# Kernel optimization log

Hardware: AMD Instinct MI355X
Metric: run time of the kernel (lower is better)

## Reference

```python
import jax, jax.numpy as jnp
import numpy as np

N, E = 50000, 800000
D, H, C, ED = 128, 8, 16, 4  # embed_dim, heads, head_dim, edge_dim


def _add_self_loops(edge_index, ea, n):
    # PyG add_self_loops with fill_value='mean': self-loop edge_attr is the
    # mean of incoming edge attributes per destination node (0 if none).
    src, dst = edge_index[0], edge_index[1]
    deg = jax.ops.segment_sum(jnp.ones((src.shape[0],), ea.dtype), dst, num_segments=n)
    loop_ea = jax.ops.segment_sum(ea, dst, num_segments=n) / jnp.maximum(deg, 1.0)[:, None]
    ar = jnp.arange(n, dtype=src.dtype)
    return (jnp.concatenate([src, ar]), jnp.concatenate([dst, ar]),
            jnp.concatenate([ea, loop_ea], axis=0))


def _gatv2(x, src, dst, ea, Wl, bl, Wr, br, We, att, bias, concat):
    n = x.shape[0]
    xl = (x @ Wl + bl).reshape(n, H, C)   # lin_l -> messages (source)
    xr = (x @ Wr + br).reshape(n, H, C)   # lin_r -> target
    e = (ea @ We).reshape(-1, H, C)       # lin_edge (no bias in PyG)
    m = jax.nn.leaky_relu(xl[src] + xr[dst] + e, negative_slope=0.2)  # [Etot,H,C]
    alpha = jnp.einsum('ehc,hc->eh', m, att)
    amax = jax.ops.segment_max(alpha, dst, num_segments=n)   # every node has a self loop
    ex = jnp.exp(alpha - amax[dst])
    den = jax.ops.segment_sum(ex, dst, num_segments=n)
    a = ex / den[dst]                                        # segment softmax over dst
    out = jax.ops.segment_sum(xl[src] * a[:, :, None], dst, num_segments=n)  # [N,H,C]
    out = out.reshape(n, H * C) if concat else out.mean(axis=1)
    return out + bias


def _ln(h, g, b):
    mu = h.mean(-1, keepdims=True)
    var = jnp.var(h, axis=-1, keepdims=True)
    return (h - mu) / jnp.sqrt(var + 1e-5) * g + b


def setup_inputs() -> dict:
    key = jax.random.key(0)
    ks = jax.random.split(key, 32)
    s = 0.05
    inp = {
        'x': jax.random.normal(ks[0], (N, D), jnp.float32),
        'edge_index': jax.random.randint(ks[1], (2, E), 0, N, jnp.int32),
        'edge_attr': jax.random.normal(ks[2], (E, ED), jnp.float32),
    }
    dims = [(D, H * C), (H * C, H * C), (H * C, C)]  # (in_dim, bias_dim per layer)
    k = 3
    for i, (din, bdim) in enumerate(dims):
        inp[f'Wl{i}'] = jax.random.normal(ks[k], (din, H * C), jnp.float32) * s; k += 1
        inp[f'bl{i}'] = jnp.zeros((H * C,), jnp.float32)
        inp[f'Wr{i}'] = jax.random.normal(ks[k], (din, H * C), jnp.float32) * s; k += 1
        inp[f'br{i}'] = jnp.zeros((H * C,), jnp.float32)
        inp[f'We{i}'] = jax.random.normal(ks[k], (ED, H * C), jnp.float32) * s; k += 1
        inp[f'att{i}'] = jax.random.normal(ks[k], (H, C), jnp.float32) * s; k += 1
        inp[f'b{i}'] = jnp.zeros((bdim,), jnp.float32)
        inp[f'g{i}'] = jnp.ones((bdim,), jnp.float32)
        inp[f'be{i}'] = jnp.zeros((bdim,), jnp.float32)
    inp['Wout'] = jax.random.normal(ks[k], (C, D), jnp.float32) * s
    inp['bout'] = jnp.zeros((D,), jnp.float32)
    return inp


def reference(x, edge_index, edge_attr,
              Wl0, bl0, Wr0, br0, We0, att0, b0, g0, be0,
              Wl1, bl1, Wr1, br1, We1, att1, b1, g1, be1,
              Wl2, bl2, Wr2, br2, We2, att2, b2, g2, be2,
              Wout, bout):
    n = x.shape[0]
    src, dst, ea = _add_self_loops(edge_index, edge_attr, n)
    layers = [
        (Wl0, bl0, Wr0, br0, We0, att0, b0, g0, be0, True),
        (Wl1, bl1, Wr1, br1, We1, att1, b1, g1, be1, True),
        (Wl2, bl2, Wr2, br2, We2, att2, b2, g2, be2, False),
    ]
    for (Wl, bl, Wr, br, We, att, bias, g, be, concat) in layers:
        h = _gatv2(x, src, dst, ea, Wl, bl, Wr, br, We, att, bias, concat)
        h = jax.nn.elu(h)
        h = _ln(h, g, be)
        if h.shape == x.shape:  # residual (layers 0,1)
            h = h + x
        x = h
    return x @ Wout + bout
```

## Files before the change

### kernel.cpp

```cpp
#include <hip/hip_runtime.h>
#include <hip/hip_bf16.h>

#define ND 128
#define NH 8
#define NC 16

typedef float v2f __attribute__((ext_vector_type(2)));
typedef short bf16x8 __attribute__((ext_vector_type(8)));
typedef float f32x4 __attribute__((ext_vector_type(4)));

static inline size_t alignup(size_t x){ return (x + 255) & ~size_t(255); }

__device__ __forceinline__ ushort f2bf(float f){
    __hip_bfloat16 h = __float2bfloat16(f);
    return *reinterpret_cast<ushort*>(&h);
}

__device__ __forceinline__ v2f unpack_bf2(uint u){
    v2f r;
    r.x = __uint_as_float(u << 16);
    r.y = __uint_as_float(u & 0xffff0000u);
    return r;
}

__device__ __forceinline__ v2f lrelu2(v2f z){
    v2f s = z * 0.2f;
    v2f r;
    r.x = fmaxf(z.x, s.x);
    r.y = fmaxf(z.y, s.y);
    return r;
}

__device__ __forceinline__ float hred8(float x){
    int y;
    y = __builtin_amdgcn_mov_dpp(__float_as_int(x), 0xB1, 0xF, 0xF, true);
    x += __int_as_float(y);
    y = __builtin_amdgcn_mov_dpp(__float_as_int(x), 0x4E, 0xF, 0xF, true);
    x += __int_as_float(y);
    y = __builtin_amdgcn_mov_dpp(__float_as_int(x), 0x141, 0xF, 0xF, true);
    x += __int_as_float(y);
    return x;
}


struct WSrc { const float* p[6]; };

#define WTHREADS (6 * 16384)

__global__ void prep_kernel(WSrc s, ushort* __restrict__ wt,
                            const int* __restrict__ dsts, int* __restrict__ deg, int E)
{
    int id = blockIdx.x * blockDim.x + threadIdx.x;
    if (id < WTHREADS) {
        int m = id >> 14;
        int r = id & 16383;
        int n = r >> 7, k = r & 127;
        wt[(size_t)m * 16384 + n * 128 + k] = f2bf(s.p[m][k * 128 + n]);
    } else {
        int e4 = (id - WTHREADS) * 4;
        if (e4 + 3 < E) {
            int4 d = *(const int4*)(dsts + e4);
            atomicAdd(&deg[d.x], 1);
            atomicAdd(&deg[d.y], 1);
            atomicAdd(&deg[d.z], 1);
            atomicAdd(&deg[d.w], 1);
        } else if (e4 < E) {
            for (int e = e4; e < E; ++e) atomicAdd(&deg[dsts[e]], 1);
        }
    }
}

__global__ __launch_bounds__(1024) void scan_kernel(const int* __restrict__ deg,
                                                    int* __restrict__ rowstart, int n)
{
    __shared__ int wsum[16];
    int tid = threadIdx.x;
    int lane = tid & 63, wid = tid >> 6;
    int carry = 0;
    for (int base = 0; base < n; base += 4096) {
        int idx = base + tid * 4;
        int4 d = make_int4(0, 0, 0, 0);
        if (idx + 3 < n) d = *(const int4*)(deg + idx);
        else {
            if (idx < n)     d.x = deg[idx];
            if (idx + 1 < n) d.y = deg[idx + 1];
            if (idx + 2 < n) d.z = deg[idx + 2];
        }
        int p0 = (d.x + 3) & ~3, p1 = (d.y + 3) & ~3;
        int p2 = (d.z + 3) & ~3, p3 = (d.w + 3) & ~3;
        int tsum = p0 + p1 + p2 + p3;
        int s = tsum;
        #pragma unroll
        for (int o = 1; o < 64; o <<= 1) {
            int t = __shfl_up(s, o);
            if (lane >= o) s += t;
        }
        if (lane == 63) wsum[wid] = s;
        __syncthreads();
        int off = carry;
        #pragma unroll
        for (int w = 0; w < 16; ++w) {
            int ws_ = wsum[w];
            if (w < wid) off += ws_;
        }
        int total = 0;
        #pragma unroll
        for (int w = 0; w < 16; ++w) total += wsum[w];
        int excl = off + (s - tsum);
        if (idx < n)     rowstart[idx]     = excl;
        if (idx + 1 < n) rowstart[idx + 1] = excl + p0;
        if (idx + 2 < n) rowstart[idx + 2] = excl + p0 + p1;
        if (idx + 3 < n) rowstart[idx + 3] = excl + p0 + p1 + p2;
        carry += total;
        __syncthreads();
    }
    if (tid == 0) rowstart[n] = carry;
}

__global__ void scatter_kernel(const int* __restrict__ srcs, const int* __restrict__ dsts,
                               const float4* __restrict__ ea4,
                               const int* __restrict__ rowstart, const int* __restrict__ deg,
                               int* __restrict__ cursor, uint4* __restrict__ recs, int E, int n)
{
    int id = blockIdx.x * blockDim.x + threadIdx.x;
    if (id < E) {
        int d = dsts[id];
        int pos = rowstart[d] + atomicAdd(&cursor[d], 1);
        float4 a = ea4[id];
        recs[pos] = make_uint4((uint)(srcs[id] << 8),
                               (uint)f2bf(a.x) | ((uint)f2bf(a.y) << 16),
                               (uint)f2bf(a.z) | ((uint)f2bf(a.w) << 16), 0u);
    } else if (id < E + n) {
        int v = id - E;
        int d = deg[v];
        int p = rowstart[v] + d;
        int pe = rowstart[v] + ((d + 3) & ~3);
        for (; p < pe; ++p) recs[p] = make_uint4(0u, 0u, 0u, 0u);
    } else if (id < E + n + 96) {
        int p = rowstart[n] + (id - E - n);
        recs[p] = make_uint4(0u, 0u, 0u, 0u);
    }
}

__global__ void easum_kernel(const int* __restrict__ rowstart, const int* __restrict__ deg,
                             const uint4* __restrict__ recs, float4* __restrict__ easum, int n)
{
    int v = blockIdx.x * blockDim.x + threadIdx.x;
    if (v >= n) return;
    int p0 = rowstart[v], d = deg[v];
    float sx = 0.f, sy = 0.f, sz = 0.f, sw = 0.f;
    for (int p = p0; p < p0 + d; ++p) {
        uint4 a = recs[p];
        sx += __uint_as_float(a.y << 16);
        sy += __uint_as_float(a.y & 0xffff0000u);
        sz += __uint_as_float(a.z << 16);
        sw += __uint_as_float(a.z & 0xffff0000u);
    }
    float inv = 1.0f / (float)(d > 0 ? d : 1);
    easum[v] = make_float4(sx * inv, sy * inv, sz * inv, sw * inv);
}


__global__ __launch_bounds__(256) void gemm_mfma(
    const float* __restrict__ X,
    const ushort* __restrict__ WTl, const float* __restrict__ bl,
    const ushort* __restrict__ WTr, const float* __restrict__ br,
    ushort* __restrict__ XLB, ushort* __restrict__ XRB, int nrows)
{
    __shared__ ushort xhi[64][136];
    __shared__ ushort xlo[64][136];
    int tid = threadIdx.x;
    int row0 = blockIdx.x * 64;

    const float4* X4 = (const float4*)X;
    #pragma unroll
    for (int i = tid; i < 64*32; i += 256) {
        int r = i >> 5, c = i & 31;
        float4 v = make_float4(0.f, 0.f, 0.f, 0.f);
        if (row0 + r < nrows) v = X4[(size_t)(row0 + r) * 32 + c];
        ushort4 h, l;
        h.x = f2bf(v.x); l.x = f2bf(v.x - __uint_as_float((uint)h.x << 16));
        h.y = f2bf(v.y); l.y = f2bf(v.y - __uint_as_float((uint)h.y << 16));
        h.z = f2bf(v.z); l.z = f2bf(v.z - __uint_as_float((uint)h.z << 16));
        h.w = f2bf(v.w); l.w = f2bf(v.w - __uint_as_float((uint)h.w << 16));
        *(ushort4*)&xhi[r][c * 4] = h;
        *(ushort4*)&xlo[r][c * 4] = l;
    }
    __syncthreads();

    int lane = tid & 63;
    int wid = tid >> 6;
    int c15 = lane & 15;
    int kblk = lane >> 4;
    int rowb = wid * 16;

    f32x4 accl[8], accr[8];
    #pragma unroll
    for (int nt = 0; nt < 8; ++nt) {
        float bvl = bl[nt * 16 + c15];
        float bvr = br[nt * 16 + c15];
        accl[nt] = (f32x4){bvl, bvl, bvl, bvl};
        accr[nt] = (f32x4){bvr, bvr, bvr, bvr};
    }

    const bf16x8* WL8 = (const bf16x8*)WTl;
    const bf16x8* WR8 = (const bf16x8*)WTr;

    #pragma unroll
    for (int kc = 0; kc < 4; ++kc) {
        int k0 = kc * 32 + kblk * 8;
        bf16x8 ahi = *(const bf16x8*)&xhi[rowb + c15][k0];
        bf16x8 alo = *(const bf16x8*)&xlo[rowb + c15][k0];
        int kidx = k0 >> 3;
        #pragma unroll
        for (int nt = 0; nt < 8; ++nt) {
            int bi = (nt * 16 + c15) * 16 + kidx;
            bf16x8 bfl = WL8[bi];
            bf16x8 bfr = WR8[bi];
            accl[nt] = __builtin_amdgcn_mfma_f32_16x16x32_bf16(ahi, bfl, accl[nt], 0, 0, 0);
            accl[nt] = __builtin_amdgcn_mfma_f32_16x16x32_bf16(alo, bfl, accl[nt], 0, 0, 0);
            accr[nt] = __builtin_amdgcn_mfma_f32_16x16x32_bf16(ahi, bfr, accr[nt], 0, 0, 0);
            accr[nt] = __builtin_amdgcn_mfma_f32_16x16x32_bf16(alo, bfr, accr[nt], 0, 0, 0);
        }
    }

    int crow = rowb + (lane >> 4) * 4;
    #pragma unroll
    for (int j = 0; j < 4; ++j) {
        int row = row0 + crow + j;
        if (row < nrows) {
            #pragma unroll
            for (int nt = 0; nt < 8; ++nt) {
                XLB[(size_t)row * 128 + nt * 16 + c15] = f2bf(accl[nt][j]);
                XRB[(size_t)row * 128 + nt * 16 + c15] = f2bf(accr[nt][j]);
            }
        }
    }
}


__device__ __forceinline__ void gat_wave(
    int dstv, int t,
    const uint* __restrict__ xl_u, const uint* __restrict__ xr_u,
    const int* __restrict__ rowstart, const int* __restrict__ deg,
    const uint4* __restrict__ recs, const float4* __restrict__ easum,
    const float* __restrict__ We, const float* __restrict__ att,
    v2f& r_out, float& l_out)
{
    v2f we0  = ((const v2f*)(We))[t];
    v2f we1  = ((const v2f*)(We + ND))[t];
    v2f we2  = ((const v2f*)(We + 2*ND))[t];
    v2f we3  = ((const v2f*)(We + 3*ND))[t];
    v2f attv = ((const v2f*)att)[t] * 1.44269504f;
    v2f xrv  = unpack_bf2(xr_u[(((uint)dstv) << 6) + t]);

    int p0 = __builtin_amdgcn_readfirstlane(rowstart[dstv]);
    int dv = __builtin_amdgcn_readfirstlane(deg[dstv]);
    int nb = (dv + 3) >> 2;

    uint xsw = xl_u[(((uint)dstv) << 6) + t];

    const uint4* rp = recs + p0;
    const char* xlc = (const char*)xl_u;
    uint t4 = (uint)t * 4u;

    v2f a = {0.f, 0.f};
    float lsum = 0.f;

    uint4 rA0 = rp[0],  rA1 = rp[1],  rA2 = rp[2],  rA3 = rp[3];
    uint4 rB0 = rp[4],  rB1 = rp[5],  rB2 = rp[6],  rB3 = rp[7];
    uint4 rC0 = rp[8],  rC1 = rp[9],  rC2 = rp[10], rC3 = rp[11];
    uint xA0 = *(const uint*)(xlc + (rA0.x + t4));
    uint xA1 = *(const uint*)(xlc + (rA1.x + t4));
    uint xA2 = *(const uint*)(xlc + (rA2.x + t4));
    uint xA3 = *(const uint*)(xlc + (rA3.x + t4));
    uint xB0 = *(const uint*)(xlc + (rB0.x + t4));
    uint xB1 = *(const uint*)(xlc + (rB1.x + t4));
    uint xB2 = *(const uint*)(xlc + (rB2.x + t4));
    uint xB3 = *(const uint*)(xlc + (rB3.x + t4));

    for (int ib = 0; ib < nb; ++ib) {
        uint xC0 = *(const uint*)(xlc + (rC0.x + t4));
        uint xC1 = *(const uint*)(xlc + (rC1.x + t4));
        uint xC2 = *(const uint*)(xlc + (rC2.x + t4));
        uint xC3 = *(const uint*)(xlc + (rC3.x + t4));
        uint4 rD0 = rp[ib*4 + 12], rD1 = rp[ib*4 + 13];
        uint4 rD2 = rp[ib*4 + 14], rD3 = rp[ib*4 + 15];

        float e0x = __uint_as_float(rA0.y << 16), e0y = __uint_as_float(rA0.y & 0xffff0000u);
        float e0z = __uint_as_float(rA0.z << 16), e0w = __uint_as_float(rA0.z & 0xffff0000u);
        float e1x = __uint_as_float(rA1.y << 16), e1y = __uint_as_float(rA1.y & 0xffff0000u);
        float e1z = __uint_as_float(rA1.z << 16), e1w = __uint_as_float(rA1.z & 0xffff0000u);
        float e2x = __uint_as_float(rA2.y << 16), e2y = __uint_as_float(rA2.y & 0xffff0000u);
        float e2z = __uint_as_float(rA2.z << 16), e2w = __uint_as_float(rA2.z & 0xffff0000u);
        float e3x = __uint_as_float(rA3.y << 16), e3y = __uint_as_float(rA3.y & 0xffff0000u);
        float e3z = __uint_as_float(rA3.z << 16), e3w = __uint_as_float(rA3.z & 0xffff0000u);

        v2f b0 = xrv + we0*e0x + we1*e0y + we2*e0z + we3*e0w;
        v2f b1 = xrv + we0*e1x + we1*e1y + we2*e1z + we3*e1w;
        v2f b2 = xrv + we0*e2x + we1*e2y + we2*e2z + we3*e2w;
        v2f b3 = xrv + we0*e3x + we1*e3y + we2*e3z + we3*e3w;

        v2f x0 = unpack_bf2(xA0);
        v2f x1 = unpack_bf2(xA1);
        v2f x2 = unpack_bf2(xA2);
        v2f x3 = unpack_bf2(xA3);

        v2f l0 = lrelu2(x0 + b0);
        v2f l1 = lrelu2(x1 + b1);
        v2f l2 = lrelu2(x2 + b2);
        v2f l3 = lrelu2(x3 + b3);

        v2f q0 = l0 * attv;
        v2f q1 = l1 * attv;
        v2f q2 = l2 * attv;
        v2f q3 = l3 * attv;
        float pt0 = q0.x + q0.y;
        float pt1 = q1.x + q1.y;
        float pt2 = q2.x + q2.y;
        float pt3 = q3.x + q3.y;

        if (ib == nb - 1) {
            int live = dv - ib*4;
            pt1 = (live > 1) ? pt1 : -1e30f;
            pt2 = (live > 2) ? pt2 : -1e30f;
            pt3 = (live > 3) ? pt3 : -1e30f;
        }

        float al0 = hred8(pt0);
        float al1 = hred8(pt1);
        float al2 = hred8(pt2);
        float al3 = hred8(pt3);

        float pe0 = exp2f(al0);
        float pe1 = exp2f(al1);
        float pe2 = exp2f(al2);
        float pe3 = exp2f(al3);
        lsum += (pe0 + pe1) + (pe2 + pe3);
        a += x0 * pe0;
        a += x1 * pe1;
        a += x2 * pe2;
        a += x3 * pe3;

        xA0 = xB0; xA1 = xB1; xA2 = xB2; xA3 = xB3;
        xB0 = xC0; xB1 = xC1; xB2 = xC2; xB3 = xC3;
        rA0 = rB0; rA1 = rB1; rA2 = rB2; rA3 = rB3;
        rB0 = rC0; rB1 = rC1; rB2 = rC2; rB3 = rC3;
        rC0 = rD0; rC1 = rD1; rC2 = rD2; rC3 = rD3;
    }

    float4 em = easum[dstv];
    v2f xs = unpack_bf2(xsw);
    v2f bs = xrv + we0*em.x + we1*em.y + we2*em.z + we3*em.w;
    v2f ls = lrelu2(xs + bs);
    v2f qs = ls * attv;
    float al = hred8(qs.x + qs.y);
    float pe = exp2f(al);
    l_out = lsum + pe;
    r_out = a + xs * pe;
}

__global__ __launch_bounds__(256) void attn_concat(
    const ushort* __restrict__ xlb, const ushort* __restrict__ xrb,
    const float* __restrict__ xin,
    const int* __restrict__ rowstart, const int* __restrict__ deg,
    const uint4* __restrict__ recs, const float4* __restrict__ easum,
    const float* __restrict__ We, const float* __restrict__ att,
    const float* __restrict__ bias, const float* __restrict__ g, const float* __restrict__ be,
    float* __restrict__ out, int n)
{
    int wid = threadIdx.x >> 6;
    int t = threadIdx.x & 63;
    int dstv = blockIdx.x * 4 + wid;
    if (dstv >= n) return;

    v2f av; float l;
    gat_wave(dstv, t, (const uint*)xlb, (const uint*)xrb, rowstart, deg, recs, easum,
             We, att, av, l);

    v2f bv = ((const v2f*)bias)[t];
    float linv = 1.0f / l;
    v2f h = av * linv + bv;
    h.x = h.x > 0.f ? h.x : (__expf(h.x) - 1.0f);
    h.y = h.y > 0.f ? h.y : (__expf(h.y) - 1.0f);

    float ss = h.x + h.y, qq = h.x*h.x + h.y*h.y;
    #pragma unroll
    for (int o = 1; o < 64; o <<= 1) { ss += __shfl_xor(ss, o); qq += __shfl_xor(qq, o); }
    float mu = ss * (1.0f / ND);
    float var = qq * (1.0f / ND) - mu * mu;
    float rstd = rsqrtf(var + 1e-5f);

    v2f gv  = ((const v2f*)g)[t];
    v2f bev = ((const v2f*)be)[t];
    v2f xiv = ((const v2f*)(xin + (size_t)dstv * ND))[t];
    v2f o2 = (h - mu) * rstd * gv + bev + xiv;
    ((v2f*)(out + (size_t)dstv * ND))[t] = o2;
}

__global__ __launch_bounds__(256) void attn_final(
    const ushort* __restrict__ xlb, const ushort* __restrict__ xrb,
    const int* __restrict__ rowstart, const int* __restrict__ deg,
    const uint4* __restrict__ recs, const float4* __restrict__ easum,
    const float* __restrict__ We, const float* __restrict__ att,
    const float* __restrict__ b2, const float* __restrict__ g2, const float* __restrict__ be2,
    const float* __restrict__ Wout, const float* __restrict__ bout,
    float* __restrict__ out, int n)
{
    __shared__ float h16s[4][16];
    int wid = threadIdx.x >> 6;
    int t = threadIdx.x & 63;
    int dstv = blockIdx.x * 4 + wid;
    if (dstv >= n) return;

    v2f av; float l;
    gat_wave(dstv, t, (const uint*)xlb, (const uint*)xrb, rowstart, deg, recs, easum,
             We, att, av, l);
    float linv = 1.0f / l;
    float v0 = av.x * linv, v1 = av.y * linv;

    #pragma unroll
    for (int o = 8; o < 64; o <<= 1) { v0 += __shfl_xor(v0, o); v1 += __shfl_xor(v1, o); }
    int cc = t & 7;
    float2 b2v = ((const float2*)b2)[cc];
    v0 = v0 * (1.0f / NH) + b2v.x;
    v1 = v1 * (1.0f / NH) + b2v.y;
    v0 = v0 > 0.f ? v0 : (__expf(v0) - 1.0f);
    v1 = v1 > 0.f ? v1 : (__expf(v1) - 1.0f);

    float ss = v0 + v1, qq = v0*v0 + v1*v1;
    #pragma unroll
    for (int o = 1; o < 8; o <<= 1) { ss += __shfl_xor(ss, o); qq += __shfl_xor(qq, o); }
    float mu = ss * (1.0f / NC);
    float var = qq * (1.0f / NC) - mu * mu;
    float rstd = rsqrtf(var + 1e-5f);
    float2 g2v = ((const float2*)g2)[cc];
    float2 be2v = ((const float2*)be2)[cc];
    float t0 = (v0 - mu) * rstd * g2v.x + be2v.x;
    float t1 = (v1 - mu) * rstd * g2v.y + be2v.y;

    if (t < 8) { h16s[wid][2*t] = t0; h16s[wid][2*t + 1] = t1; }

    float2 ov = ((const float2*)bout)[t];
    #pragma unroll
    for (int k = 0; k < NC; k++) {
        float hk = h16s[wid][k];
        float2 wv = ((const float2*)Wout)[k * 64 + t];
        ov.x = fmaf(hk, wv.x, ov.x);
        ov.y = fmaf(hk, wv.y, ov.y);
    }
    ((float2*)(out + (size_t)dstv * ND))[t] = ov;
}


extern "C" void kernel_launch(void* const* d_in, const int* in_sizes, int n_in,
                              void* d_out, int out_size, void* d_ws, size_t ws_size,
                              hipStream_t stream)
{
    const float* x_in = (const float*)d_in[0];
    const int*   ei   = (const int*)d_in[1];
    const float* ea   = (const float*)d_in[2];
    const int N = in_sizes[0] / ND;
    const int E = in_sizes[1] / 2;
    const int* srcs = ei;
    const int* dsts = ei + E;
    const float4* ea4 = (const float4*)ea;

    const float *Wl[3], *bl[3], *Wr[3], *br[3], *We[3], *att[3], *bb[3], *gg[3], *be[3];
    for (int l = 0; l < 3; l++) {
        int b = 3 + 9 * l;
        Wl[l]  = (const float*)d_in[b + 0];
        bl[l]  = (const float*)d_in[b + 1];
        Wr[l]  = (const float*)d_in[b + 2];
        br[l]  = (const float*)d_in[b + 3];
        We[l]  = (const float*)d_in[b + 4];
        att[l] = (const float*)d_in[b + 5];
        bb[l]  = (const float*)d_in[b + 6];
        gg[l]  = (const float*)d_in[b + 7];
        be[l]  = (const float*)d_in[b + 8];
    }
    const float* Wout = (const float*)d_in[30];
    const float* bout = (const float*)d_in[31];

    const size_t EP = (size_t)E + 3 * (size_t)N + 96;

    char* ws = (char*)d_ws;
    size_t off = 0;
    int* deg        = (int*)(ws + off);      off = alignup(off + (size_t)N * 4);
    int* cursor     = (int*)(ws + off);      off = alignup(off + (size_t)N * 4);
    size_t zero_bytes = off;
    int* rowstart   = (int*)(ws + off);      off = alignup(off + (size_t)(N + 1) * 4);
    uint4* recs     = (uint4*)(ws + off);    off = alignup(off + EP * 16);
    float4* easum   = (float4*)(ws + off);   off = alignup(off + (size_t)N * 16);
    ushort* xlb     = (ushort*)(ws + off);   off = alignup(off + (size_t)N * ND * 2);
    ushort* xrb     = (ushort*)(ws + off);   off = alignup(off + (size_t)N * ND * 2);
    float* xa       = (float*)(ws + off);    off = alignup(off + (size_t)N * ND * 4);
    ushort* wt      = (ushort*)(ws + off);   off = alignup(off + (size_t)6 * 16384 * 2);
    float* xb       = (float*)d_out;

    hipMemsetAsync(d_ws, 0, zero_bytes, stream);

    WSrc wsrc;
    wsrc.p[0] = Wl[0]; wsrc.p[1] = Wr[0];
    wsrc.p[2] = Wl[1]; wsrc.p[3] = Wr[1];
    wsrc.p[4] = Wl[2]; wsrc.p[5] = Wr[2];

    int pthreads = WTHREADS + (E + 3) / 4;
    prep_kernel<<<(pthreads + 255) / 256, 256, 0, stream>>>(wsrc, wt, dsts, deg, E);
    scan_kernel<<<1, 1024, 0, stream>>>(deg, rowstart, N);
    int sthreads = E + N + 96;
    scatter_kernel<<<(sthreads + 255) / 256, 256, 0, stream>>>(srcs, dsts, ea4, rowstart, deg,
                                                               cursor, recs, E, N);
    easum_kernel<<<(N + 255) / 256, 256, 0, stream>>>(rowstart, deg, recs, easum, N);

    int gblocks = (N + 63) / 64;
    int ablocks = (N + 3) / 4;

    const ushort* WT0l = wt;
    const ushort* WT0r = wt + 16384;
    const ushort* WT1l = wt + 2 * 16384;
    const ushort* WT1r = wt + 3 * 16384;
    const ushort* WT2l = wt + 4 * 16384;
    const ushort* WT2r = wt + 5 * 16384;

    gemm_mfma<<<gblocks, 256, 0, stream>>>(x_in, WT0l, bl[0], WT0r, br[0], xlb, xrb, N);
    attn_concat<<<ablocks, 256, 0, stream>>>(xlb, xrb, x_in, rowstart, deg, recs, easum,
                                             We[0], att[0], bb[0], gg[0], be[0], xa, N);
    gemm_mfma<<<gblocks, 256, 0, stream>>>(xa, WT1l, bl[1], WT1r, br[1], xlb, xrb, N);
    attn_concat<<<ablocks, 256, 0, stream>>>(xlb, xrb, xa, rowstart, deg, recs, easum,
                                             We[1], att[1], bb[1], gg[1], be[1], xb, N);
    gemm_mfma<<<gblocks, 256, 0, stream>>>(xb, WT2l, bl[2], WT2r, br[2], xlb, xrb, N);
    attn_final<<<ablocks, 256, 0, stream>>>(xlb, xrb, rowstart, deg, recs, easum,
                                            We[2], att[2], bb[2], gg[2], be[2],
                                            Wout, bout, (float*)d_out, N);
}
```

Baseline: 418.9 us.

## Fuse self-loop edge-attr mean into first attention pass and deepen gather prefetch

Removes the separate easum kernel. The first attention layer now accumulates the per-destination mean of incoming edge attributes while it streams the edge records, and writes it out for the later layers to read. The gather pipeline is also restructured: source indices are prefetched as single words one stage further ahead, giving three stages of xl gathers in flight instead of two. This saves a launch and a pass over the records, at the cost of more registers and some extra arithmetic in layer 0.

```diff
diff --git a/kernel.cpp b/kernel.cpp
--- a/kernel.cpp
+++ b/kernel.cpp
@@ -142,24 +142,6 @@
     }
 }
 
-__global__ void easum_kernel(const int* __restrict__ rowstart, const int* __restrict__ deg,
-                             const uint4* __restrict__ recs, float4* __restrict__ easum, int n)
-{
-    int v = blockIdx.x * blockDim.x + threadIdx.x;
-    if (v >= n) return;
-    int p0 = rowstart[v], d = deg[v];
-    float sx = 0.f, sy = 0.f, sz = 0.f, sw = 0.f;
-    for (int p = p0; p < p0 + d; ++p) {
-        uint4 a = recs[p];
-        sx += __uint_as_float(a.y << 16);
-        sy += __uint_as_float(a.y & 0xffff0000u);
-        sz += __uint_as_float(a.z << 16);
-        sw += __uint_as_float(a.z & 0xffff0000u);
-    }
-    float inv = 1.0f / (float)(d > 0 ? d : 1);
-    easum[v] = make_float4(sx * inv, sy * inv, sz * inv, sw * inv);
-}
-
 
 __global__ __launch_bounds__(256) void gemm_mfma(
     const float* __restrict__ X,
@@ -239,11 +221,12 @@
 }
 
 
+template<bool CE>
 __device__ __forceinline__ void gat_wave(
     int dstv, int t,
     const uint* __restrict__ xl_u, const uint* __restrict__ xr_u,
     const int* __restrict__ rowstart, const int* __restrict__ deg,
-    const uint4* __restrict__ recs, const float4* __restrict__ easum,
+    const uint4* __restrict__ recs, float4* __restrict__ easum,
     const float* __restrict__ We, const float* __restrict__ att,
     v2f& r_out, float& l_out)
 {
@@ -261,31 +244,40 @@
     uint xsw = xl_u[(((uint)dstv) << 6) + t];
 
     const uint4* rp = recs + p0;
+    const uint* rpw = (const uint*)rp;
     const char* xlc = (const char*)xl_u;
     uint t4 = (uint)t * 4u;
 
     v2f a = {0.f, 0.f};
     float lsum = 0.f;
-
-    uint4 rA0 = rp[0],  rA1 = rp[1],  rA2 = rp[2],  rA3 = rp[3];
-    uint4 rB0 = rp[4],  rB1 = rp[5],  rB2 = rp[6],  rB3 = rp[7];
-    uint4 rC0 = rp[8],  rC1 = rp[9],  rC2 = rp[10], rC3 = rp[11];
-    uint xA0 = *(const uint*)(xlc + (rA0.x + t4));
-    uint xA1 = *(const uint*)(xlc + (rA1.x + t4));
-    uint xA2 = *(const uint*)(xlc + (rA2.x + t4));
-    uint xA3 = *(const uint*)(xlc + (rA3.x + t4));
-    uint xB0 = *(const uint*)(xlc + (rB0.x + t4));
-    uint xB1 = *(const uint*)(xlc + (rB1.x + t4));
-    uint xB2 = *(const uint*)(xlc + (rB2.x + t4));
-    uint xB3 = *(const uint*)(xlc + (rB3.x + t4));
+    float ssx = 0.f, ssy = 0.f, ssz = 0.f, ssw = 0.f;
+
+    uint4 rA0 = rp[0], rA1 = rp[1], rA2 = rp[2], rA3 = rp[3];
+    uint4 rB0 = rp[4], rB1 = rp[5], rB2 = rp[6], rB3 = rp[7];
+    uint sC0 = rpw[32], sC1 = rpw[36], sC2 = rpw[40], sC3 = rpw[44];
+    uint sD0 = rpw[48], sD1 = rpw[52], sD2 = rpw[56], sD3 = rpw[60];
+    uint gA0 = *(const uint*)(xlc + (rA0.x + t4));
+    uint gA1 = *(const uint*)(xlc + (rA1.x + t4));
+    uint gA2 = *(const uint*)(xlc + (rA2.x + t4));
+    uint gA3 = *(const uint*)(xlc + (rA3.x + t4));
+    uint gB0 = *(const uint*)(xlc + (rB0.x + t4));
+    uint gB1 = *(const uint*)(xlc + (rB1.x + t4));
+    uint gB2 = *(const uint*)(xlc + (rB2.x + t4));
+    uint gB3 = *(const uint*)(xlc + (rB3.x + t4));
+    uint gC0 = *(const uint*)(xlc + (sC0 + t4));
+    uint gC1 = *(const uint*)(xlc + (sC1 + t4));
+    uint gC2 = *(const uint*)(xlc + (sC2 + t4));
+    uint gC3 = *(const uint*)(xlc + (sC3 + t4));
 
     for (int ib = 0; ib < nb; ++ib) {
-        uint xC0 = *(const uint*)(xlc + (rC0.x + t4));
-        uint xC1 = *(const uint*)(xlc + (rC1.x + t4));
-        uint xC2 = *(const uint*)(xlc + (rC2.x + t4));
-        uint xC3 = *(const uint*)(xlc + (rC3.x + t4));
-        uint4 rD0 = rp[ib*4 + 12], rD1 = rp[ib*4 + 13];
-        uint4 rD2 = rp[ib*4 + 14], rD3 = rp[ib*4 + 15];
+        uint gD0 = *(const uint*)(xlc + (sD0 + t4));
+        uint gD1 = *(const uint*)(xlc + (sD1 + t4));
+        uint gD2 = *(const uint*)(xlc + (sD2 + t4));
+        uint gD3 = *(const uint*)(xlc + (sD3 + t4));
+        int wbase = (ib + 4) * 16;
+        uint sE0 = rpw[wbase], sE1 = rpw[wbase + 4], sE2 = rpw[wbase + 8], sE3 = rpw[wbase + 12];
+        int rbase = (ib + 2) * 4;
+        uint4 rC0 = rp[rbase], rC1 = rp[rbase + 1], rC2 = rp[rbase + 2], rC3 = rp[rbase + 3];
 
         float e0x = __uint_as_float(rA0.y << 16), e0y = __uint_as_float(rA0.y & 0xffff0000u);
         float e0z = __uint_as_float(rA0.z << 16), e0w = __uint_as_float(rA0.z & 0xffff0000u);
@@ -296,15 +288,22 @@
         float e3x = __uint_as_float(rA3.y << 16), e3y = __uint_as_float(rA3.y & 0xffff0000u);
         float e3z = __uint_as_float(rA3.z << 16), e3w = __uint_as_float(rA3.z & 0xffff0000u);
 
+        if (CE) {
+            ssx += (e0x + e1x) + (e2x + e3x);
+            ssy += (e0y + e1y) + (e2y + e3y);
+            ssz += (e0z + e1z) + (e2z + e3z);
+            ssw += (e0w + e1w) + (e2w + e3w);
+        }
+
         v2f b0 = xrv + we0*e0x + we1*e0y + we2*e0z + we3*e0w;
         v2f b1 = xrv + we0*e1x + we1*e1y + we2*e1z + we3*e1w;
         v2f b2 = xrv + we0*e2x + we1*e2y + we2*e2z + we3*e2w;
         v2f b3 = xrv + we0*e3x + we1*e3y + we2*e3z + we3*e3w;
 
-        v2f x0 = unpack_bf2(xA0);
-        v2f x1 = unpack_bf2(xA1);
-        v2f x2 = unpack_bf2(xA2);
-        v2f x3 = unpack_bf2(xA3);
+        v2f x0 = unpack_bf2(gA0);
+        v2f x1 = unpack_bf2(gA1);
+        v2f x2 = unpack_bf2(gA2);
+        v2f x3 = unpack_bf2(gA3);
 
         v2f l0 = lrelu2(x0 + b0);
         v2f l1 = lrelu2(x1 + b1);
@@ -342,14 +341,22 @@
         a += x2 * pe2;
         a += x3 * pe3;
 
-        xA0 = xB0; xA1 = xB1; xA2 = xB2; xA3 = xB3;
-        xB0 = xC0; xB1 = xC1; xB2 = xC2; xB3 = xC3;
+        gA0 = gB0; gA1 = gB1; gA2 = gB2; gA3 = gB3;
+        gB0 = gC0; gB1 = gC1; gB2 = gC2; gB3 = gC3;
+        gC0 = gD0; gC1 = gD1; gC2 = gD2; gC3 = gD3;
         rA0 = rB0; rA1 = rB1; rA2 = rB2; rA3 = rB3;
         rB0 = rC0; rB1 = rC1; rB2 = rC2; rB3 = rC3;
-        rC0 = rD0; rC1 = rD1; rC2 = rD2; rC3 = rD3;
-    }
-
-    float4 em = easum[dstv];
+        sD0 = sE0; sD1 = sE1; sD2 = sE2; sD3 = sE3;
+    }
+
+    float4 em;
+    if (CE) {
+        float inv = 1.0f / (float)(dv > 0 ? dv : 1);
+        em = make_float4(ssx * inv, ssy * inv, ssz * inv, ssw * inv);
+        if (t == 0) easum[dstv] = em;
+    } else {
+        em = easum[dstv];
+    }
     v2f xs = unpack_bf2(xsw);
     v2f bs = xrv + we0*em.x + we1*em.y + we2*em.z + we3*em.w;
     v2f ls = lrelu2(xs + bs);
@@ -360,11 +367,12 @@
     r_out = a + xs * pe;
 }
 
+template<bool CE>
 __global__ __launch_bounds__(256) void attn_concat(
     const ushort* __restrict__ xlb, const ushort* __restrict__ xrb,
     const float* __restrict__ xin,
     const int* __restrict__ rowstart, const int* __restrict__ deg,
-    const uint4* __restrict__ recs, const float4* __restrict__ easum,
+    const uint4* __restrict__ recs, float4* __restrict__ easum,
     const float* __restrict__ We, const float* __restrict__ att,
     const float* __restrict__ bias, const float* __restrict__ g, const float* __restrict__ be,
     float* __restrict__ out, int n)
@@ -375,8 +383,8 @@
     if (dstv >= n) return;
 
     v2f av; float l;
-    gat_wave(dstv, t, (const uint*)xlb, (const uint*)xrb, rowstart, deg, recs, easum,
-             We, att, av, l);
+    gat_wave<CE>(dstv, t, (const uint*)xlb, (const uint*)xrb, rowstart, deg, recs, easum,
+                 We, att, av, l);
 
     v2f bv = ((const v2f*)bias)[t];
     float linv = 1.0f / l;
@@ -401,7 +409,7 @@
 __global__ __launch_bounds__(256) void attn_final(
     const ushort* __restrict__ xlb, const ushort* __restrict__ xrb,
     const int* __restrict__ rowstart, const int* __restrict__ deg,
-    const uint4* __restrict__ recs, const float4* __restrict__ easum,
+    const uint4* __restrict__ recs, float4* __restrict__ easum,
     const float* __restrict__ We, const float* __restrict__ att,
     const float* __restrict__ b2, const float* __restrict__ g2, const float* __restrict__ be2,
     const float* __restrict__ Wout, const float* __restrict__ bout,
@@ -414,8 +422,8 @@
     if (dstv >= n) return;
 
     v2f av; float l;
-    gat_wave(dstv, t, (const uint*)xlb, (const uint*)xrb, rowstart, deg, recs, easum,
-             We, att, av, l);
+    gat_wave<false>(dstv, t, (const uint*)xlb, (const uint*)xrb, rowstart, deg, recs, easum,
+                    We, att, av, l);
     float linv = 1.0f / l;
     float v0 = av.x * linv, v1 = av.y * linv;
 
@@ -511,7 +519,6 @@
     int sthreads = E + N + 96;
     scatter_kernel<<<(sthreads + 255) / 256, 256, 0, stream>>>(srcs, dsts, ea4, rowstart, deg,
                                                                cursor, recs, E, N);
-    easum_kernel<<<(N + 255) / 256, 256, 0, stream>>>(rowstart, deg, recs, easum, N);
 
     int gblocks = (N + 63) / 64;
     int ablocks = (N + 3) / 4;
@@ -524,11 +531,11 @@
     const ushort* WT2r = wt + 5 * 16384;
 
     gemm_mfma<<<gblocks, 256, 0, stream>>>(x_in, WT0l, bl[0], WT0r, br[0], xlb, xrb, N);
-    attn_concat<<<ablocks, 256, 0, stream>>>(xlb, xrb, x_in, rowstart, deg, recs, easum,
-                                             We[0], att[0], bb[0], gg[0], be[0], xa, N);
+    attn_concat<true><<<ablocks, 256, 0, stream>>>(xlb, xrb, x_in, rowstart, deg, recs, easum,
+                                                   We[0], att[0], bb[0], gg[0], be[0], xa, N);
     gemm_mfma<<<gblocks, 256, 0, stream>>>(xa, WT1l, bl[1], WT1r, br[1], xlb, xrb, N);
-    attn_concat<<<ablocks, 256, 0, stream>>>(xlb, xrb, xa, rowstart, deg, recs, easum,
-                                             We[1], att[1], bb[1], gg[1], be[1], xb, N);
+    attn_concat<false><<<ablocks, 256, 0, stream>>>(xlb, xrb, xa, rowstart, deg, recs, easum,
+                                                    We[1], att[1], bb[1], gg[1], be[1], xb, N);
     gemm_mfma<<<gblocks, 256, 0, stream>>>(xb, WT2l, bl[2], WT2r, br[2], xlb, xrb, N);
     attn_final<<<ablocks, 256, 0, stream>>>(xlb, xrb, rowstart, deg, recs, easum,
                                             We[2], att[2], bb[2], gg[2], be[2],
```

New measurement: 430.3 us. 1.03x slower.
